# Optimization experiments

Hardware: AMD Instinct MI355X
Metric: run time of the kernel (lower is better)

Reference implementation:

```python
import jax, jax.numpy as jnp
import numpy as np

B, D_IN, H = 16384, 512, 1024


def setup_inputs() -> dict:
    key = jax.random.key(0)
    ks = jax.random.split(key, 12)
    s_in = 1.0 / np.sqrt(D_IN)
    s_h = 1.0 / np.sqrt(H)
    d = {
        "input_x": jax.random.normal(ks[0], (B, D_IN), jnp.float32),
        "h_old": jax.random.normal(ks[1], (B, H), jnp.float32),
        "c_old": jax.random.normal(ks[2], (B, H), jnp.float32),
    }
    names_U = ["Ui", "Uf", "Uo", "Uc"]
    names_W = ["Wi", "Wf", "Wo", "Wc"]
    for i, n in enumerate(names_U):
        d[n + "_w"] = jax.random.normal(ks[3 + i], (D_IN, H), jnp.float32) * s_in
        d[n + "_b"] = jnp.zeros((H,), jnp.float32)
    for i, n in enumerate(names_W):
        d[n + "_w"] = jax.random.normal(ks[7 + i], (H, H), jnp.float32) * s_h
        d[n + "_b"] = jnp.zeros((H,), jnp.float32)
    return d


def reference(input_x, h_old, c_old,
              Ui_w, Ui_b, Wi_w, Wi_b,
              Uf_w, Uf_b, Wf_w, Wf_b,
              Uo_w, Uo_b, Wo_w, Wo_b,
              Uc_w, Uc_b, Wc_w, Wc_b):
    # Fuse the 8 small GEMMs into 2: concatenate gate projections along the
    # output dim (math identical to 8 separate Dense layers + adds).
    U = jnp.concatenate([Ui_w, Uf_w, Uo_w, Uc_w], axis=1)   # [D_in, 4H]
    W = jnp.concatenate([Wi_w, Wf_w, Wo_w, Wc_w], axis=1)   # [H, 4H]
    b = jnp.concatenate([Ui_b + Wi_b, Uf_b + Wf_b, Uo_b + Wo_b, Uc_b + Wc_b])
    gates = input_x @ U + h_old @ W + b                      # [B, 4H]
    i_t, f_t, o_t, g_t = jnp.split(gates, 4, axis=1)
    i_t = jax.nn.sigmoid(i_t)
    f_t = jax.nn.sigmoid(f_t)
    o_t = jax.nn.sigmoid(o_t)
    c_t = jnp.tanh(g_t)
    c = i_t * c_t + f_t * c_old
    h_new = o_t * jnp.tanh(c)
    return (h_new, c)
```

## Files before the change

kernel.cpp:

```cpp
#include <hip/hip_runtime.h>
#include <hip/hip_bf16.h>
#include <stdint.h>

#define B_ROWS 16384
#define D_IN   512
#define H_DIM  1024
#define K_TOT  1536
#define NKT    48
#define NIT    12

typedef __attribute__((ext_vector_type(8)))  short bf16x8;
typedef __attribute__((ext_vector_type(16))) float f32x16;
typedef __attribute__((ext_vector_type(4)))  float float4v;
typedef __attribute__((ext_vector_type(8)))  unsigned short u16x8;

__device__ __forceinline__ unsigned short f2bf(float f) {
    uint32_t u = __float_as_uint(f);
    u = (u + 0x7FFFu + ((u >> 16) & 1u)) >> 16;
    return (unsigned short)u;
}

__global__ void cvt_A(const float* __restrict__ x, const float* __restrict__ h,
                      unsigned short* __restrict__ Ag) {
    int t     = blockIdx.x * blockDim.x + threadIdx.x;
    int lane  = t & 63;
    int chunk = (t >> 6) & 15;
    int rest  = t >> 10;
    int tile  = rest % 48;
    int bm    = rest / 48;
    int row   = bm * 256 + (chunk >> 1) * 32 + (lane & 31);
    int k     = tile * 32 + (chunk & 1) * 16 + (lane >> 5) * 8;
    const float* src = (k < 512) ? (x + (size_t)row * D_IN + k)
                                 : (h + (size_t)row * H_DIM + (k - 512));
    float4v v0 = *(const float4v*)(src);
    float4v v1 = *(const float4v*)(src + 4);
    u16x8 o;
    o[0] = f2bf(v0[0]); o[1] = f2bf(v0[1]); o[2] = f2bf(v0[2]); o[3] = f2bf(v0[3]);
    o[4] = f2bf(v1[0]); o[5] = f2bf(v1[1]); o[6] = f2bf(v1[2]); o[7] = f2bf(v1[3]);
    *(u16x8*)(Ag + (size_t)t * 8) = o;
}

__global__ void cvt_B(const float* __restrict__ Ui, const float* __restrict__ Uf,
                      const float* __restrict__ Uo, const float* __restrict__ Uc,
                      const float* __restrict__ Wi, const float* __restrict__ Wf,
                      const float* __restrict__ Wo, const float* __restrict__ Wc,
                      unsigned short* __restrict__ Bg) {
    int t     = blockIdx.x * blockDim.x + threadIdx.x;
    int lane  = t & 63;
    int chunk = (t >> 6) & 15;
    int rest  = t >> 10;
    int tile  = rest % 48;
    int bn    = rest / 48;
    int c     = bn * 256 + (chunk >> 1) * 32 + (lane & 31);
    int g     = (c >> 5) & 3;
    int hcol  = ((c >> 7) << 5) | (c & 31);
    int k     = tile * 32 + (chunk & 1) * 16 + (lane >> 5) * 8;
    const float* up = (g == 0) ? Ui : (g == 1) ? Uf : (g == 2) ? Uo : Uc;
    const float* wp = (g == 0) ? Wi : (g == 1) ? Wf : (g == 2) ? Wo : Wc;
    u16x8 o;
    if (k < 512) {
        const float* s = up + (size_t)k * H_DIM + hcol;
        #pragma unroll
        for (int i = 0; i < 8; ++i) o[i] = f2bf(s[(size_t)i * H_DIM]);
    } else {
        const float* s = wp + (size_t)(k - 512) * H_DIM + hcol;
        #pragma unroll
        for (int i = 0; i < 8; ++i) o[i] = f2bf(s[(size_t)i * H_DIM]);
    }
    *(u16x8*)(Bg + (size_t)t * 8) = o;
}

__global__ void cvt_bias(const float* __restrict__ Uib, const float* __restrict__ Ufb,
                         const float* __restrict__ Uob, const float* __restrict__ Ucb,
                         const float* __restrict__ Wib, const float* __restrict__ Wfb,
                         const float* __restrict__ Wob, const float* __restrict__ Wcb,
                         float* __restrict__ bias) {
    int t = blockIdx.x * blockDim.x + threadIdx.x;
    int g = t >> 10, h = t & 1023;
    const float* ub = (g == 0) ? Uib : (g == 1) ? Ufb : (g == 2) ? Uob : Ucb;
    const float* wb = (g == 0) ? Wib : (g == 1) ? Wfb : (g == 2) ? Wob : Wcb;
    bias[t] = ub[h] + wb[h];
}

__global__ __launch_bounds__(512, 2) void lstm_gemm(
        const unsigned short* __restrict__ Ag, const unsigned short* __restrict__ Bg,
        const float* __restrict__ bias, const float* __restrict__ c_old,
        float* __restrict__ out) {
    __shared__ __align__(1024) char lds[131072];

    const int tid = threadIdx.x;
    const int l   = tid & 63;
    const int wv  = tid >> 6;
    const int wm  = wv >> 1;
    const int wn  = wv & 1;

    const int orig = blockIdx.x;
    const int xcd  = orig & 7;
    const int jj   = orig >> 3;
    const int bn   = (xcd & 3) * 4 + (jj & 3);
    const int bm   = (xcd >> 2) * 32 + (jj >> 2);

    const unsigned short* aT = Ag + (size_t)(wv * 2) * 512 + l * 8;
    const unsigned short* bT = Bg + (size_t)(wv * 2) * 512 + l * 8;
    const size_t aTileBase = (size_t)bm * 48 * 8192;
    const size_t bTileBase = (size_t)bn * 48 * 8192;

#define GLDS(SRC, DST) __builtin_amdgcn_global_load_lds(                            \
        (const __attribute__((address_space(1))) void*)(SRC),                       \
        (__attribute__((address_space(3))) void*)(DST), 16, 0, 0)

#define STAGE(ST, SLOT) do {                                                        \
    const unsigned short* _a = aT + aTileBase + (size_t)(ST) * 8192;                \
    const unsigned short* _b = bT + bTileBase + (size_t)(ST) * 8192;                \
    char* _da = (char*)lds + (SLOT) * 32768 + (wv * 2) * 1024;                      \
    char* _db = _da + 16384;                                                        \
    GLDS(_a,       _da);        GLDS(_a + 512, _da + 1024);                         \
    GLDS(_b,       _db);        GLDS(_b + 512, _db + 1024);                         \
} while (0)

    f32x16 acc[2][4] = {};

#define PHASE(P, ST) do {                                                           \
    const char* _Ab = (const char*)lds + (P) * 32768 + wm * 4096 + l * 16;          \
    const char* _Bb = (const char*)lds + (P) * 32768 + 16384 + wn * 8192 + l * 16;  \
    bf16x8 aF[2][2], bF[4][2];                                                      \
    _Pragma("unroll") for (int mm = 0; mm < 2; ++mm)                                \
        _Pragma("unroll") for (int ks = 0; ks < 2; ++ks)                            \
            aF[mm][ks] = *(const bf16x8*)(_Ab + mm * 2048 + ks * 1024);             \
    _Pragma("unroll") for (int nn = 0; nn < 4; ++nn)                                \
        _Pragma("unroll") for (int ks = 0; ks < 2; ++ks)                            \
            bF[nn][ks] = *(const bf16x8*)(_Bb + nn * 2048 + ks * 1024);             \
    STAGE(ST, ((P) + 3) & 3);                                                       \
    __builtin_amdgcn_s_setprio(1);                                                  \
    _Pragma("unroll") for (int ks = 0; ks < 2; ++ks)                                \
        _Pragma("unroll") for (int mm = 0; mm < 2; ++mm)                            \
            _Pragma("unroll") for (int nn = 0; nn < 4; ++nn)                        \
                acc[mm][nn] = __builtin_amdgcn_mfma_f32_32x32x16_bf16(              \
                    aF[mm][ks], bF[nn][ks], acc[mm][nn], 0, 0, 0);                  \
    __builtin_amdgcn_s_setprio(0);                                                  \
    asm volatile("s_waitcnt vmcnt(8)\ns_barrier" ::: "memory");                     \
} while (0)

    STAGE(0, 0); STAGE(1, 1); STAGE(2, 2);
    asm volatile("s_waitcnt vmcnt(8)\ns_barrier" ::: "memory");

    #pragma unroll 1
    for (int i = 0; i < NIT; ++i) {
        const int b4 = i * 4;
        int s0 = b4 + 3;
        int s1 = b4 + 4; if (s1 >= NKT) s1 -= NKT;
        int s2 = b4 + 5; if (s2 >= NKT) s2 -= NKT;
        int s3 = b4 + 6; if (s3 >= NKT) s3 -= NKT;
        PHASE(0, s0);
        PHASE(1, s1);
        PHASE(2, s2);
        PHASE(3, s3);
    }
    asm volatile("s_waitcnt vmcnt(0)" ::: "memory");

    const int r31 = l & 31;
    const int h5  = l >> 5;
    const int hh  = (bn * 2 + wn) * 32 + r31;
    const float bi  = bias[hh];
    const float bff = bias[1024 + hh];
    const float bo  = bias[2048 + hh];
    const float bc  = bias[3072 + hh];

    #pragma unroll
    for (int mm = 0; mm < 2; ++mm) {
        const int rb = bm * 256 + wm * 64 + mm * 32 + 4 * h5;
        #pragma unroll
        for (int r = 0; r < 16; ++r) {
            const int row = rb + (r & 3) + 8 * (r >> 2);
            float iv = acc[mm][0][r] + bi;
            float fv = acc[mm][1][r] + bff;
            float ov = acc[mm][2][r] + bo;
            float gv = acc[mm][3][r] + bc;
            float it = 1.f / (1.f + __expf(-iv));
            float ft = 1.f / (1.f + __expf(-fv));
            float ot = 1.f / (1.f + __expf(-ov));
            float gt = 1.f - 2.f / (1.f + __expf(2.f * gv));
            float co = c_old[(size_t)row * H_DIM + hh];
            float cn = it * gt + ft * co;
            float th = 1.f - 2.f / (1.f + __expf(2.f * cn));
            out[(size_t)row * H_DIM + hh] = ot * th;
            out[(size_t)B_ROWS * H_DIM + (size_t)row * H_DIM + hh] = cn;
        }
    }
#undef PHASE
#undef STAGE
#undef GLDS
}

extern "C" void kernel_launch(void* const* d_in, const int* in_sizes, int n_in,
                              void* d_out, int out_size, void* d_ws, size_t ws_size,
                              hipStream_t stream) {
    const float* x  = (const float*)d_in[0];
    const float* h0 = (const float*)d_in[1];
    const float* c0 = (const float*)d_in[2];
    const float* Uw[4] = {(const float*)d_in[3],  (const float*)d_in[5],
                          (const float*)d_in[7],  (const float*)d_in[9]};
    const float* Ub[4] = {(const float*)d_in[4],  (const float*)d_in[6],
                          (const float*)d_in[8],  (const float*)d_in[10]};
    const float* Ww[4] = {(const float*)d_in[11], (const float*)d_in[13],
                          (const float*)d_in[15], (const float*)d_in[17]};
    const float* Wb[4] = {(const float*)d_in[12], (const float*)d_in[14],
                          (const float*)d_in[16], (const float*)d_in[18]};

    unsigned short* Ag = (unsigned short*)d_ws;
    unsigned short* Bg = Ag + (size_t)B_ROWS * K_TOT;
    float* bias        = (float*)(Bg + (size_t)4096 * K_TOT);
    float* out         = (float*)d_out;

    cvt_A<<<12288, 256, 0, stream>>>(x, h0, Ag);
    cvt_B<<<3072, 256, 0, stream>>>(Uw[0], Uw[1], Uw[2], Uw[3],
                                    Ww[0], Ww[1], Ww[2], Ww[3], Bg);
    cvt_bias<<<16, 256, 0, stream>>>(Ub[0], Ub[1], Ub[2], Ub[3],
                                     Wb[0], Wb[1], Wb[2], Wb[3], bias);
    lstm_gemm<<<1024, 512, 0, stream>>>(Ag, Bg, bias, c0, out);
}
```

Measured before the change: 274.1 us.

## Shrink GEMM tiles to 128x128 with 16x16 MFMA and triple-buffered LDS

Changes the block tile from 256x256 (512 threads) to 128x128 (256 threads) with four workgroups per CU, switching from 32x32x16 to 16x16x32 bf16 MFMA and from a 4-slot to a 3-slot LDS ring. The pre-swizzled A/B workspace layouts in the convert kernels are rewritten to match the new 16-row fragment ordering. The intent is to raise occupancy and wave count for latency hiding and to spread work across more blocks. In exchange, per-tile arithmetic intensity drops, so more global traffic is needed to re-read A and B, and prefetch depth is shallower.

```diff
diff --git a/kernel.cpp b/kernel.cpp
--- a/kernel.cpp
+++ b/kernel.cpp
@@ -7,10 +7,9 @@
 #define H_DIM  1024
 #define K_TOT  1536
 #define NKT    48
-#define NIT    12
 
 typedef __attribute__((ext_vector_type(8)))  short bf16x8;
-typedef __attribute__((ext_vector_type(16))) float f32x16;
+typedef __attribute__((ext_vector_type(4)))  float f32x4;
 typedef __attribute__((ext_vector_type(4)))  float float4v;
 typedef __attribute__((ext_vector_type(8)))  unsigned short u16x8;
 
@@ -24,12 +23,12 @@
                       unsigned short* __restrict__ Ag) {
     int t     = blockIdx.x * blockDim.x + threadIdx.x;
     int lane  = t & 63;
-    int chunk = (t >> 6) & 15;
-    int rest  = t >> 10;
+    int chunk = (t >> 6) & 7;
+    int rest  = t >> 9;
     int tile  = rest % 48;
     int bm    = rest / 48;
-    int row   = bm * 256 + (chunk >> 1) * 32 + (lane & 31);
-    int k     = tile * 32 + (chunk & 1) * 16 + (lane >> 5) * 8;
+    int row   = bm * 128 + chunk * 16 + (lane & 15);
+    int k     = tile * 32 + (lane >> 4) * 8;
     const float* src = (k < 512) ? (x + (size_t)row * D_IN + k)
                                  : (h + (size_t)row * H_DIM + (k - 512));
     float4v v0 = *(const float4v*)(src);
@@ -47,14 +46,14 @@
                       unsigned short* __restrict__ Bg) {
     int t     = blockIdx.x * blockDim.x + threadIdx.x;
     int lane  = t & 63;
-    int chunk = (t >> 6) & 15;
-    int rest  = t >> 10;
+    int chunk = (t >> 6) & 7;
+    int rest  = t >> 9;
     int tile  = rest % 48;
     int bn    = rest / 48;
-    int c     = bn * 256 + (chunk >> 1) * 32 + (lane & 31);
-    int g     = (c >> 5) & 3;
-    int hcol  = ((c >> 7) << 5) | (c & 31);
-    int k     = tile * 32 + (chunk & 1) * 16 + (lane >> 5) * 8;
+    int c     = bn * 128 + chunk * 16 + (lane & 15);
+    int g     = (c >> 4) & 3;
+    int hcol  = ((c >> 6) << 4) | (c & 15);
+    int k     = tile * 32 + (lane >> 4) * 8;
     const float* up = (g == 0) ? Ui : (g == 1) ? Uf : (g == 2) ? Uo : Uc;
     const float* wp = (g == 0) ? Wi : (g == 1) ? Wf : (g == 2) ? Wo : Wc;
     u16x8 o;
@@ -82,11 +81,11 @@
     bias[t] = ub[h] + wb[h];
 }
 
-__global__ __launch_bounds__(512, 2) void lstm_gemm(
+__global__ __launch_bounds__(256, 4) void lstm_gemm(
         const unsigned short* __restrict__ Ag, const unsigned short* __restrict__ Bg,
         const float* __restrict__ bias, const float* __restrict__ c_old,
         float* __restrict__ out) {
-    __shared__ __align__(1024) char lds[131072];
+    __shared__ __align__(1024) char lds[49152];
 
     const int tid = threadIdx.x;
     const int l   = tid & 63;
@@ -96,95 +95,86 @@
 
     const int orig = blockIdx.x;
     const int xcd  = orig & 7;
-    const int jj   = orig >> 3;
-    const int bn   = (xcd & 3) * 4 + (jj & 3);
-    const int bm   = (xcd >> 2) * 32 + (jj >> 2);
-
-    const unsigned short* aT = Ag + (size_t)(wv * 2) * 512 + l * 8;
-    const unsigned short* bT = Bg + (size_t)(wv * 2) * 512 + l * 8;
-    const size_t aTileBase = (size_t)bm * 48 * 8192;
-    const size_t bTileBase = (size_t)bn * 48 * 8192;
+    const int j    = orig >> 3;
+    const int bn   = xcd * 4 + (j & 3);
+    const int bm   = j >> 2;
+
+    const unsigned short* aCur = Ag + ((size_t)bm * 48 * 8 + 2 * wv) * 512 + l * 8;
+    const unsigned short* bCur = Bg + ((size_t)bn * 48 * 8 + 2 * wv) * 512 + l * 8;
+
+    const int aRd = wm * 4096 + l * 16;
+    const int bRd = 8192 + wn * 4096 + l * 16;
 
 #define GLDS(SRC, DST) __builtin_amdgcn_global_load_lds(                            \
         (const __attribute__((address_space(1))) void*)(SRC),                       \
         (__attribute__((address_space(3))) void*)(DST), 16, 0, 0)
 
-#define STAGE(ST, SLOT) do {                                                        \
-    const unsigned short* _a = aT + aTileBase + (size_t)(ST) * 8192;                \
-    const unsigned short* _b = bT + bTileBase + (size_t)(ST) * 8192;                \
-    char* _da = (char*)lds + (SLOT) * 32768 + (wv * 2) * 1024;                      \
-    char* _db = _da + 16384;                                                        \
-    GLDS(_a,       _da);        GLDS(_a + 512, _da + 1024);                         \
-    GLDS(_b,       _db);        GLDS(_b + 512, _db + 1024);                         \
+#define STAGE(SLOTBASE) do {                                                        \
+    char* _da = (char*)lds + (SLOTBASE) + wv * 2048;                                \
+    GLDS(aCur, _da);            GLDS(aCur + 512, _da + 1024);                       \
+    GLDS(bCur, _da + 8192);     GLDS(bCur + 512, _da + 8192 + 1024);                \
+    aCur += 4096; bCur += 4096;                                                     \
 } while (0)
 
-    f32x16 acc[2][4] = {};
-
-#define PHASE(P, ST) do {                                                           \
-    const char* _Ab = (const char*)lds + (P) * 32768 + wm * 4096 + l * 16;          \
-    const char* _Bb = (const char*)lds + (P) * 32768 + 16384 + wn * 8192 + l * 16;  \
-    bf16x8 aF[2][2], bF[4][2];                                                      \
-    _Pragma("unroll") for (int mm = 0; mm < 2; ++mm)                                \
-        _Pragma("unroll") for (int ks = 0; ks < 2; ++ks)                            \
-            aF[mm][ks] = *(const bf16x8*)(_Ab + mm * 2048 + ks * 1024);             \
-    _Pragma("unroll") for (int nn = 0; nn < 4; ++nn)                                \
-        _Pragma("unroll") for (int ks = 0; ks < 2; ++ks)                            \
-            bF[nn][ks] = *(const bf16x8*)(_Bb + nn * 2048 + ks * 1024);             \
-    STAGE(ST, ((P) + 3) & 3);                                                       \
+    f32x4 acc[4][4] = {};
+
+#define PHASE(SLOT) do {                                                            \
+    const char* _b = (const char*)lds + (SLOT) * 16384;                             \
+    bf16x8 aF[4], bF[4];                                                            \
+    _Pragma("unroll") for (int m = 0; m < 4; ++m)                                   \
+        aF[m] = *(const bf16x8*)(_b + aRd + m * 1024);                              \
+    _Pragma("unroll") for (int n = 0; n < 4; ++n)                                   \
+        bF[n] = *(const bf16x8*)(_b + bRd + n * 1024);                              \
+    STAGE(((((SLOT) + 2) % 3)) * 16384);                                            \
     __builtin_amdgcn_s_setprio(1);                                                  \
-    _Pragma("unroll") for (int ks = 0; ks < 2; ++ks)                                \
-        _Pragma("unroll") for (int mm = 0; mm < 2; ++mm)                            \
-            _Pragma("unroll") for (int nn = 0; nn < 4; ++nn)                        \
-                acc[mm][nn] = __builtin_amdgcn_mfma_f32_32x32x16_bf16(              \
-                    aF[mm][ks], bF[nn][ks], acc[mm][nn], 0, 0, 0);                  \
+    _Pragma("unroll") for (int m = 0; m < 4; ++m)                                   \
+        _Pragma("unroll") for (int n = 0; n < 4; ++n)                               \
+            acc[m][n] = __builtin_amdgcn_mfma_f32_16x16x32_bf16(                    \
+                aF[m], bF[n], acc[m][n], 0, 0, 0);                                  \
     __builtin_amdgcn_s_setprio(0);                                                  \
-    asm volatile("s_waitcnt vmcnt(8)\ns_barrier" ::: "memory");                     \
+    asm volatile("s_waitcnt vmcnt(4)\ns_barrier" ::: "memory");                     \
 } while (0)
 
-    STAGE(0, 0); STAGE(1, 1); STAGE(2, 2);
-    asm volatile("s_waitcnt vmcnt(8)\ns_barrier" ::: "memory");
+    STAGE(0); STAGE(16384);
+    asm volatile("s_waitcnt vmcnt(4)\ns_barrier" ::: "memory");
 
     #pragma unroll 1
-    for (int i = 0; i < NIT; ++i) {
-        const int b4 = i * 4;
-        int s0 = b4 + 3;
-        int s1 = b4 + 4; if (s1 >= NKT) s1 -= NKT;
-        int s2 = b4 + 5; if (s2 >= NKT) s2 -= NKT;
-        int s3 = b4 + 6; if (s3 >= NKT) s3 -= NKT;
-        PHASE(0, s0);
-        PHASE(1, s1);
-        PHASE(2, s2);
-        PHASE(3, s3);
+    for (int i = 0; i < 15; ++i) {
+        PHASE(0);
+        PHASE(1);
+        PHASE(2);
     }
+    PHASE(0);
+    aCur -= (size_t)48 * 4096;  bCur -= (size_t)48 * 4096;
+    PHASE(1);
+    PHASE(2);
     asm volatile("s_waitcnt vmcnt(0)" ::: "memory");
 
-    const int r31 = l & 31;
-    const int h5  = l >> 5;
-    const int hh  = (bn * 2 + wn) * 32 + r31;
+    const int hh  = bn * 32 + wn * 16 + (l & 15);
     const float bi  = bias[hh];
     const float bff = bias[1024 + hh];
     const float bo  = bias[2048 + hh];
     const float bc  = bias[3072 + hh];
 
     #pragma unroll
-    for (int mm = 0; mm < 2; ++mm) {
-        const int rb = bm * 256 + wm * 64 + mm * 32 + 4 * h5;
+    for (int m = 0; m < 4; ++m) {
+        const int rb = bm * 128 + wm * 64 + m * 16 + ((l >> 4) * 4);
         #pragma unroll
-        for (int r = 0; r < 16; ++r) {
-            const int row = rb + (r & 3) + 8 * (r >> 2);
-            float iv = acc[mm][0][r] + bi;
-            float fv = acc[mm][1][r] + bff;
-            float ov = acc[mm][2][r] + bo;
-            float gv = acc[mm][3][r] + bc;
+        for (int jj = 0; jj < 4; ++jj) {
+            const int r = rb + jj;
+            float iv = acc[m][0][jj] + bi;
+            float fv = acc[m][1][jj] + bff;
+            float ov = acc[m][2][jj] + bo;
+            float gv = acc[m][3][jj] + bc;
             float it = 1.f / (1.f + __expf(-iv));
             float ft = 1.f / (1.f + __expf(-fv));
             float ot = 1.f / (1.f + __expf(-ov));
             float gt = 1.f - 2.f / (1.f + __expf(2.f * gv));
-            float co = c_old[(size_t)row * H_DIM + hh];
+            float co = c_old[(size_t)r * H_DIM + hh];
             float cn = it * gt + ft * co;
             float th = 1.f - 2.f / (1.f + __expf(2.f * cn));
-            out[(size_t)row * H_DIM + hh] = ot * th;
-            out[(size_t)B_ROWS * H_DIM + (size_t)row * H_DIM + hh] = cn;
+            out[(size_t)r * H_DIM + hh] = ot * th;
+            out[(size_t)B_ROWS * H_DIM + (size_t)r * H_DIM + hh] = cn;
         }
     }
 #undef PHASE
@@ -217,5 +207,5 @@
                                     Ww[0], Ww[1], Ww[2], Ww[3], Bg);
     cvt_bias<<<16, 256, 0, stream>>>(Ub[0], Ub[1], Ub[2], Ub[3],
                                      Wb[0], Wb[1], Wb[2], Wb[3], bias);
-    lstm_gemm<<<1024, 512, 0, stream>>>(Ag, Bg, bias, c0, out);
-}
+    lstm_gemm<<<4096, 256, 0, stream>>>(Ag, Bg, bias, c0, out);
+}
```

Result: slower. 285.2 us (+4.0%).
